# Kernel tuning notes

Hardware: AMD Instinct MI355X
Metric: run time of the kernel (lower is better)

The kernel has to match this reference:

```python
import jax, jax.numpy as jnp
import numpy as np

N, K, A, LOCAL, PAIR = 1024, 48, 5, 512, 128
RBF_BINS = 16

def _normalize(v, eps=1e-8):
    return v / jnp.sqrt(jnp.sum(v * v, axis=-1, keepdims=True) + eps)

def _frames(pos):
    # pos: (N, A, 3); backbone frame from N(0), CA(1), C(2) via Gram-Schmidt
    n, ca, c = pos[:, 0], pos[:, 1], pos[:, 2]
    e1 = _normalize(c - ca)
    v2 = n - ca
    e2 = _normalize(v2 - jnp.sum(v2 * e1, -1, keepdims=True) * e1)
    e3 = jnp.cross(e1, e2)
    R = jnp.stack([e1, e2, e3], axis=-1)  # (N,3,3) columns are frame axes
    return R, ca

def _rbf(d, d_min=0.0, d_max=22.0, bins=RBF_BINS):
    centers = jnp.linspace(d_min, d_max, bins)
    step = (d_max - d_min) / bins
    return jnp.exp(-((d[..., None] - centers) / step) ** 2)

def setup_inputs():
    key = jax.random.key(0)
    ks = jax.random.split(key, 16)
    def rn(k, shape, scale=1.0):
        return (scale * jax.random.normal(k, shape)).astype(jnp.float32)
    local = rn(ks[0], (N, LOCAL))
    pos = rn(ks[1], (N, A, 3), 3.0)
    pair = rn(ks[2], (N, N, PAIR), 0.1)
    neighbours = jax.random.randint(ks[3], (N, K), 0, N).astype(jnp.int32)
    mask = jnp.ones((N,), dtype=bool)
    d_dist = A * A * RBF_BINS   # 400
    d_dir = A * A * 3           # 75
    d_vec = 2 * A * 3           # 30
    s = lambda f: 1.0 / np.sqrt(f)
    return dict(
        local=local, pos=pos, pair=pair, neighbours=neighbours, mask=mask,
        W_li=rn(ks[4], (LOCAL, PAIR), s(LOCAL)),
        W_lj=rn(ks[5], (LOCAL, PAIR), s(LOCAL)),
        W_dist=rn(ks[6], (d_dist, PAIR), s(d_dist)),
        W_dir=rn(ks[7], (d_dir, PAIR), s(d_dir)),
        W_rot=rn(ks[8], (9, PAIR), s(9)),
        W_vec=rn(ks[9], (d_vec, PAIR), s(d_vec)),
        ln_scale=jnp.ones((PAIR,), jnp.float32),
        ln_bias=jnp.zeros((PAIR,), jnp.float32),
        mlp_w1=rn(ks[10], (PAIR, 2 * PAIR), s(PAIR)),
        mlp_b1=jnp.zeros((2 * PAIR,), jnp.float32),
        mlp_w2=rn(ks[11], (2 * PAIR, PAIR), s(2 * PAIR)),
        mlp_b2=jnp.zeros((PAIR,), jnp.float32),
    )

def reference(local, pos, pair, neighbours, mask,
              W_li, W_lj, W_dist, W_dir, W_rot, W_vec,
              ln_scale, ln_bias, mlp_w1, mlp_b1, mlp_w2, mlp_b2):
    n_idx = jnp.arange(neighbours.shape[0])
    pair_mask = (mask[:, None] & mask[neighbours]) & (neighbours != -1)
    p = pair[n_idx[:, None], neighbours]                      # (N,K,PAIR) gather
    R, t = _frames(pos)                                       # (N,3,3), (N,3)
    pos_nb = pos[neighbours]                                  # (N,K,A,3)
    # source / target node feature projections
    p = p + (local @ W_li)[:, None] + (local @ W_lj)[neighbours]
    # distance features: all atom-pair distances, RBF-encoded in [0, 22]
    off = pos[:, None, :, None, :] - pos_nb[:, :, None, :, :] # (N,K,A,A,3)
    dist = jnp.sqrt(jnp.sum(off * off, -1) + 1e-8)            # (N,K,A,A)
    p = p + _rbf(dist).reshape(*neighbours.shape, -1) @ W_dist
    # direction features: atom-pair offsets in the local frame, normalized
    off_local = jnp.einsum('nij,nkabi->nkabj', R, off)
    p = p + _normalize(off_local).reshape(*neighbours.shape, -1) @ W_dir
    # relative rotation features: R_i^T R_j, flattened
    R_rel = jnp.einsum('nai,nkaj->nkij', R, R[neighbours])
    p = p + R_rel.reshape(*neighbours.shape, 9) @ W_rot
    # pair vector features: self and neighbour atoms in the local frame (x0.1)
    x_self = jnp.einsum('nij,nai->naj', R, pos - t[:, None])            # (N,A,3)
    x_nb = jnp.einsum('nij,nkai->nkaj', R, pos_nb - t[:, None, None])   # (N,K,A,3)
    vec = jnp.concatenate(
        (0.1 * jnp.broadcast_to(x_self[:, None], x_nb.shape), 0.1 * x_nb),
        axis=-1).reshape(*neighbours.shape, -1)
    p = p + vec @ W_vec
    # LayerNorm (scale + offset)
    mu = jnp.mean(p, -1, keepdims=True)
    var = jnp.var(p, -1, keepdims=True)
    p = (p - mu) * jax.lax.rsqrt(var + 1e-5) * ln_scale + ln_bias
    # MLP: hidden 2*PAIR, gelu, linear out
    p = jax.nn.gelu(p @ mlp_w1 + mlp_b1) @ mlp_w2 + mlp_b2
    return p, pair_mask
```

## Files before the change

kernel.cpp:

```cpp
#include <hip/hip_runtime.h>
#include <hip/hip_bf16.h>
#include <math.h>

#define N 1024
#define K 48
#define A 5
#define LOCALD 512
#define PAIRD 128
#define ROWS 32
#define FEATK 544
#define SF_STRIDE_B 1152

#define WS_LI (N*9 + N*3 + N*15)
#define WS_LJ (WS_LI + N*128)
#define WCT_OFF 1159168u
#define W1T_OFF 1298432u
#define W2T_OFF 1363968u

typedef _Float16 half8 __attribute__((ext_vector_type(8)));
typedef float f32x16 __attribute__((ext_vector_type(16)));

__device__ __forceinline__ float gelu_fast(float x) {
    float u2 = 1.5957691216057308f * x * (1.0f + 0.044715f * x * x);
    float t = __expf(-u2);
    return x * __builtin_amdgcn_rcpf(1.0f + t);
}

__device__ __forceinline__ void frame_from(const float* __restrict__ P, float* __restrict__ R) {
    float e1x = P[6] - P[3], e1y = P[7] - P[4], e1z = P[8] - P[5];
    float inv1 = rsqrtf(e1x * e1x + e1y * e1y + e1z * e1z + 1e-8f);
    e1x *= inv1; e1y *= inv1; e1z *= inv1;
    float v2x = P[0] - P[3], v2y = P[1] - P[4], v2z = P[2] - P[5];
    float dp = v2x * e1x + v2y * e1y + v2z * e1z;
    float e2x = v2x - dp * e1x, e2y = v2y - dp * e1y, e2z = v2z - dp * e1z;
    float inv2 = rsqrtf(e2x * e2x + e2y * e2y + e2z * e2z + 1e-8f);
    e2x *= inv2; e2y *= inv2; e2z *= inv2;
    float e3x = e1y * e2z - e1z * e2y;
    float e3y = e1z * e2x - e1x * e2z;
    float e3z = e1x * e2y - e1y * e2x;
    R[0] = e1x; R[1] = e2x; R[2] = e3x;
    R[3] = e1y; R[4] = e2y; R[5] = e3y;
    R[6] = e1z; R[7] = e2z; R[8] = e3z;
}

__global__ __launch_bounds__(256) void prep_kernel(
    const float* __restrict__ local_,
    const float* __restrict__ W_li, const float* __restrict__ W_lj,
    const float* __restrict__ Wd, const float* __restrict__ Wdir,
    const float* __restrict__ Wrot, const float* __restrict__ Wv,
    const float* __restrict__ w1, const float* __restrict__ w2,
    float* __restrict__ ws, char* __restrict__ wsb)
{
    const int tid = threadIdx.x;
    if (blockIdx.x >= 256) {
        _Float16* wct = (_Float16*)(wsb + WCT_OFF);
        _Float16* w1t = (_Float16*)(wsb + W1T_OFF);
        _Float16* w2t = (_Float16*)(wsb + W2T_OFF);
        int g = (blockIdx.x - 256) * 256 + tid;
        if (g < 128 * 544) {
            int c = g & 127, f = g >> 7;
            float v = 0.0f;
            if (f < 400) v = Wd[(size_t)f * 128 + c];
            else if (f < 475) v = Wdir[(size_t)(f - 400) * 128 + c];
            else if (f < 484) v = Wrot[(size_t)(f - 475) * 128 + c];
            else if (f < 514) v = Wv[(size_t)(f - 484) * 128 + c];
            wct[(size_t)c * FEATK + f] = (_Float16)v;
        } else {
            int g2 = g - 128 * 544;
            if (g2 < 256 * 128) {
                int c = g2 & 255, f = g2 >> 8;
                w1t[(size_t)c * 128 + f] = (_Float16)w1[(size_t)f * 256 + c];
            } else {
                int g3 = g2 - 256 * 128;
                if (g3 < 128 * 256) {
                    int c = g3 & 127, f = g3 >> 7;
                    w2t[(size_t)c * 256 + f] = (_Float16)w2[(size_t)f * 128 + c];
                }
            }
        }
        return;
    }

    const int n0 = blockIdx.x * 4;
    __shared__ float sl[4][LOCALD];
    for (int t = tid; t < 4 * LOCALD; t += 256) {
        int r = t >> 9, q = t & 511;
        sl[r][q] = local_[(size_t)(n0 + r) * LOCALD + q];
    }
    __syncthreads();

    const int c = tid & 127;
    const int hh = tid >> 7;
    const int r0 = hh * 2;
    float ali0 = 0, ali1 = 0, alj0 = 0, alj1 = 0;
    const float* wli = W_li + c;
    const float* wlj = W_lj + c;
    #pragma unroll 8
    for (int f = 0; f < LOCALD; ++f) {
        float a_ = wli[(size_t)f * 128];
        float b_ = wlj[(size_t)f * 128];
        float l0 = sl[r0 + 0][f], l1 = sl[r0 + 1][f];
        ali0 += l0 * a_; ali1 += l1 * a_;
        alj0 += l0 * b_; alj1 += l1 * b_;
    }
    ws[WS_LI + (size_t)(n0 + r0 + 0) * 128 + c] = ali0;
    ws[WS_LI + (size_t)(n0 + r0 + 1) * 128 + c] = ali1;
    ws[WS_LJ + (size_t)(n0 + r0 + 0) * 128 + c] = alj0;
    ws[WS_LJ + (size_t)(n0 + r0 + 1) * 128 + c] = alj1;
}

__device__ __forceinline__ void sfw(char* smem, int r, int f, float v) {
    int off = r * SF_STRIDE_B + ((f * 2) ^ ((r & 7) << 4));
    *(_Float16*)(smem + off) = (_Float16)v;
}

__global__ __launch_bounds__(256, 4) void main_kernel(
    const float* __restrict__ pair, const float* __restrict__ pos,
    const int* __restrict__ neigh, const int* __restrict__ mask,
    const float* __restrict__ ln_s, const float* __restrict__ ln_b,
    const float* __restrict__ b1, const float* __restrict__ b2,
    const float* __restrict__ ws, const char* __restrict__ wsb,
    float* __restrict__ out)
{
    const int R0 = blockIdx.x * ROWS;
    const int tid = threadIdx.x;
    const int lane = tid & 63;
    const int wv = tid >> 6;
    const int myrow = lane & 31;
    const int khalf = (lane >> 5) * 8;
    const int hi = lane >> 5;
    const int swz = (myrow & 7) << 4;

    __shared__ __align__(16) char smem[40960];
    int*   sn  = (int*)(smem + 36864);
    int*   sj  = (int*)(smem + 36992);
    float* spn = (float*)(smem + 37120);
    float* spj = (float*)(smem + 39040);

    const _Float16* wct = (const _Float16*)(wsb + WCT_OFF);
    const int colbase = wv * 32 + myrow;

    if (tid < ROWS) {
        int Rg = R0 + tid;
        int n = Rg / K;
        int kk = Rg - n * K;
        int j = neigh[n * K + kk];
        if (j < 0) j += N;
        sn[tid] = n; sj[tid] = j;
    }
    __syncthreads();

    const int nb0 = R0 / K;
    const int nb1 = (nb0 + 1 < N) ? nb0 + 1 : nb0;
    float li0 = ws[WS_LI + (size_t)nb0 * PAIRD + colbase];
    float li1 = ws[WS_LI + (size_t)nb1 * PAIRD + colbase];
    float pv[16];
    #pragma unroll
    for (int q = 0; q < 16; ++q) {
        int rr = (q & 3) + 8 * (q >> 2) + 4 * hi;
        int nq = sn[rr], jq = sj[rr];
        float li = (nq == nb0) ? li0 : li1;
        pv[q] = pair[((size_t)nq * N + jq) * PAIRD + colbase]
              + ws[WS_LJ + (size_t)jq * PAIRD + colbase] + li;
    }

    for (int t = tid; t < ROWS * 15; t += 256) {
        int r = t / 15, q = t % 15;
        spn[t] = pos[(size_t)sn[r] * 15 + q];
        spj[t] = pos[(size_t)sj[r] * 15 + q];
    }
    __syncthreads();

    {
        const int fr  = tid >> 3;
        const int sub = tid & 7;
        const float* Pn = spn + fr * 15;
        const float* Pj = spj + fr * 15;

        sfw(smem, fr, 514 + sub, 0.0f);
        sfw(smem, fr, 522 + sub, 0.0f);
        sfw(smem, fr, 530 + sub, 0.0f);
        if (sub < 6) sfw(smem, fr, 538 + sub, 0.0f);

        float rn[9];
        frame_from(Pn, rn);

        #pragma unroll
        for (int m = 0; m < 4; ++m) {
            int ab = sub + 8 * m;
            if (ab < 25) {
                int a = ab / 5, b = ab - 5 * (ab / 5);
                float o0 = Pn[a * 3 + 0] - Pj[b * 3 + 0];
                float o1 = Pn[a * 3 + 1] - Pj[b * 3 + 1];
                float o2 = Pn[a * 3 + 2] - Pj[b * 3 + 2];
                float d = sqrtf(o0 * o0 + o1 * o1 + o2 * o2 + 1e-8f);
                float z = d * (16.0f / 22.0f);
                int base = a * 80 + b * 16;
                int rb = fr * SF_STRIDE_B;
                int rsw = (fr & 7) << 4;
                #pragma unroll
                for (int bp = 0; bp < 8; ++bp) {
                    float e0 = __expf(-z * z);
                    float z1 = z - 1.0666666666666667f;
                    float e1 = __expf(-z1 * z1);
                    z = z1 - 1.0666666666666667f;
                    union { _Float16 h[2]; unsigned u; } pk;
                    pk.h[0] = (_Float16)e0; pk.h[1] = (_Float16)e1;
                    int off = rb + (((base + bp * 2) * 2) ^ rsw);
                    *(unsigned*)(smem + off) = pk.u;
                }
                float l0 = rn[0] * o0 + rn[3] * o1 + rn[6] * o2;
                float l1 = rn[1] * o0 + rn[4] * o1 + rn[7] * o2;
                float l2 = rn[2] * o0 + rn[5] * o1 + rn[8] * o2;
                float inv = rsqrtf(l0 * l0 + l1 * l1 + l2 * l2 + 1e-8f);
                int dbase = 400 + a * 15 + b * 3;
                sfw(smem, fr, dbase + 0, l0 * inv);
                sfw(smem, fr, dbase + 1, l1 * inv);
                sfw(smem, fr, dbase + 2, l2 * inv);
            }
        }

        #pragma unroll
        for (int m = 0; m < 2; ++m) {
            int task = (m == 0) ? sub : (sub < 2 ? 8 + sub : -1);
            if (task >= 0) {
                int a = task >> 1;
                int kind = task & 1;
                const float* Ps = kind ? Pj : Pn;
                float v0 = Ps[a * 3 + 0] - Pn[3];
                float v1 = Ps[a * 3 + 1] - Pn[4];
                float v2 = Ps[a * 3 + 2] - Pn[5];
                float x0 = rn[0] * v0 + rn[3] * v1 + rn[6] * v2;
                float x1 = rn[1] * v0 + rn[4] * v1 + rn[7] * v2;
                float x2 = rn[2] * v0 + rn[5] * v1 + rn[8] * v2;
                int dbase = 484 + a * 6 + kind * 3;
                sfw(smem, fr, dbase + 0, 0.1f * x0);
                sfw(smem, fr, dbase + 1, 0.1f * x1);
                sfw(smem, fr, dbase + 2, 0.1f * x2);
            }
        }

        if (sub == 7) {
            float rj[9];
            frame_from(Pj, rj);
            #pragma unroll
            for (int i = 0; i < 3; ++i)
                #pragma unroll
                for (int jd = 0; jd < 3; ++jd) {
                    float v = rn[0 * 3 + i] * rj[0 * 3 + jd]
                            + rn[1 * 3 + i] * rj[1 * 3 + jd]
                            + rn[2 * 3 + i] * rj[2 * 3 + jd];
                    sfw(smem, fr, 475 + i * 3 + jd, v);
                }
        }
    }
    __syncthreads();

    f32x16 acc0, acc1;
    #pragma unroll
    for (int q = 0; q < 16; ++q) { acc0[q] = 0.0f; acc1[q] = 0.0f; }
    {
        const _Float16* wp = wct + (size_t)colbase * FEATK + khalf;
        #pragma unroll
        for (int ks = 0; ks < 34; ks += 2) {
            half8 b0 = *(const half8*)(wp + ks * 16);
            half8 b1 = *(const half8*)(wp + (ks + 1) * 16);
            int k0 = ks * 16 + khalf;
            int k1 = (ks + 1) * 16 + khalf;
            half8 a0 = *(const half8*)(smem + myrow * SF_STRIDE_B + ((k0 * 2) ^ swz));
            half8 a1 = *(const half8*)(smem + myrow * SF_STRIDE_B + ((k1 * 2) ^ swz));
            acc0 = __builtin_amdgcn_mfma_f32_32x32x16_f16(a0, b0, acc0, 0, 0, 0);
            acc1 = __builtin_amdgcn_mfma_f32_32x32x16_f16(a1, b1, acc1, 0, 0, 0);
        }
    }
    __syncthreads();

    #pragma unroll
    for (int q = 0; q < 16; ++q) {
        int rr = (q & 3) + 8 * (q >> 2) + 4 * hi;
        *(float*)(smem + rr * 512 + colbase * 4) = acc0[q] + acc1[q] + pv[q];
    }
    __syncthreads();

    {
        float lns0 = ln_s[lane], lns1 = ln_s[lane + 64];
        float lnb0 = ln_b[lane], lnb1 = ln_b[lane + 64];
        #pragma unroll
        for (int rr8 = 0; rr8 < 8; ++rr8) {
            int row = wv * 8 + rr8;
            float v0 = *(float*)(smem + row * 512 + lane * 4);
            float v1 = *(float*)(smem + row * 512 + (lane + 64) * 4);
            float s = v0 + v1, s2 = v0 * v0 + v1 * v1;
            #pragma unroll
            for (int o = 32; o > 0; o >>= 1) {
                s += __shfl_xor(s, o, 64);
                s2 += __shfl_xor(s2, o, 64);
            }
            float mu = s * (1.0f / 128.0f);
            float var = s2 * (1.0f / 128.0f) - mu * mu;
            float rs = rsqrtf(var + 1e-5f);
            int sw = (row & 7) << 4;
            *(_Float16*)(smem + 16384 + row * 256 + ((lane * 2) ^ sw)) =
                (_Float16)((v0 - mu) * rs * lns0 + lnb0);
            *(_Float16*)(smem + 16384 + row * 256 + (((lane + 64) * 2) ^ sw)) =
                (_Float16)((v1 - mu) * rs * lns1 + lnb1);
        }
    }
    __syncthreads();

    {
        const _Float16* w1t = (const _Float16*)(wsb + W1T_OFF);
        const int c0 = wv * 64 + myrow;
        const int c1 = c0 + 32;
        const _Float16* wp0 = w1t + (size_t)c0 * 128 + khalf;
        const _Float16* wp1 = w1t + (size_t)c1 * 128 + khalf;
        f32x16 h0, h1;
        #pragma unroll
        for (int q = 0; q < 16; ++q) { h0[q] = 0.0f; h1[q] = 0.0f; }
        #pragma unroll
        for (int ks = 0; ks < 8; ++ks) {
            half8 wf0 = *(const half8*)(wp0 + ks * 16);
            half8 wf1 = *(const half8*)(wp1 + ks * 16);
            int k0 = ks * 16 + khalf;
            half8 a = *(const half8*)(smem + 16384 + myrow * 256 + ((k0 * 2) ^ swz));
            h0 = __builtin_amdgcn_mfma_f32_32x32x16_f16(a, wf0, h0, 0, 0, 0);
            h1 = __builtin_amdgcn_mfma_f32_32x32x16_f16(a, wf1, h1, 0, 0, 0);
        }
        float bb0 = b1[c0], bb1 = b1[c1];
        #pragma unroll
        for (int q = 0; q < 16; ++q) {
            int rr = (q & 3) + 8 * (q >> 2) + 4 * hi;
            int sw = (rr & 7) << 4;
            *(_Float16*)(smem + rr * 512 + ((c0 * 2) ^ sw)) = (_Float16)gelu_fast(h0[q] + bb0);
            *(_Float16*)(smem + rr * 512 + ((c1 * 2) ^ sw)) = (_Float16)gelu_fast(h1[q] + bb1);
        }
    }
    __syncthreads();

    {
        const _Float16* w2t = (const _Float16*)(wsb + W2T_OFF);
        const int oc = wv * 32 + myrow;
        const _Float16* wp = w2t + (size_t)oc * 256 + khalf;
        f32x16 o0, o1;
        #pragma unroll
        for (int q = 0; q < 16; ++q) { o0[q] = 0.0f; o1[q] = 0.0f; }
        #pragma unroll
        for (int ks = 0; ks < 16; ks += 2) {
            half8 w0 = *(const half8*)(wp + ks * 16);
            half8 w1f = *(const half8*)(wp + (ks + 1) * 16);
            int k0 = ks * 16 + khalf;
            int k1 = (ks + 1) * 16 + khalf;
            half8 a0 = *(const half8*)(smem + myrow * 512 + ((k0 * 2) ^ swz));
            half8 a1 = *(const half8*)(smem + myrow * 512 + ((k1 * 2) ^ swz));
            o0 = __builtin_amdgcn_mfma_f32_32x32x16_f16(a0, w0, o0, 0, 0, 0);
            o1 = __builtin_amdgcn_mfma_f32_32x32x16_f16(a1, w1f, o1, 0, 0, 0);
        }
        float bb = b2[oc];
        #pragma unroll
        for (int q = 0; q < 16; ++q) {
            int rr = (q & 3) + 8 * (q >> 2) + 4 * hi;
            out[((size_t)(R0 + rr)) * PAIRD + oc] = o0[q] + o1[q] + bb;
        }
    }

    if (tid < ROWS) {
        int Rg = R0 + tid;
        int n = Rg / K;
        int kk = Rg - n * K;
        int jr = neigh[n * K + kk];
        int jj = jr < 0 ? jr + N : jr;
        bool pm = (jr != -1) && (mask[n] != 0) && (mask[jj] != 0);
        out[(size_t)N * K * PAIRD + Rg] = pm ? 1.0f : 0.0f;
    }
}

extern "C" void kernel_launch(void* const* d_in, const int* in_sizes, int n_in,
                              void* d_out, int out_size, void* d_ws, size_t ws_size,
                              hipStream_t stream) {
    const float* local_ = (const float*)d_in[0];
    const float* pos = (const float*)d_in[1];
    const float* pair = (const float*)d_in[2];
    const int* neigh = (const int*)d_in[3];
    const int* mask = (const int*)d_in[4];
    const float* W_li = (const float*)d_in[5];
    const float* W_lj = (const float*)d_in[6];
    const float* W_dist = (const float*)d_in[7];
    const float* W_dir = (const float*)d_in[8];
    const float* W_rot = (const float*)d_in[9];
    const float* W_vec = (const float*)d_in[10];
    const float* ln_s = (const float*)d_in[11];
    const float* ln_b = (const float*)d_in[12];
    const float* w1 = (const float*)d_in[13];
    const float* b1 = (const float*)d_in[14];
    const float* w2 = (const float*)d_in[15];
    const float* b2 = (const float*)d_in[16];
    float* ws = (float*)d_ws;
    char* wsb = (char*)d_ws;
    float* out = (float*)d_out;

    hipLaunchKernelGGL(prep_kernel, dim3(256 + 528), dim3(256), 0, stream,
                       local_, W_li, W_lj, W_dist, W_dir, W_rot, W_vec,
                       w1, w2, ws, wsb);
    hipLaunchKernelGGL(main_kernel, dim3((N * K) / ROWS), dim3(256), 0, stream,
                       pair, pos, neigh, mask, ln_s, ln_b, b1, b2, ws, wsb, out);
}
```

Measured before the change: 83.75 us.

## Split MLP into separate 64-row kernel via fp16 workspace intermediate

The fused kernel now stops after LayerNorm and writes normalized fp16 rows to a workspace buffer. A new mlp_kernel processes 64 rows per block, so each loaded weight fragment feeds two MFMA row tiles. This roughly halves weight traffic per row and lets the MLP run at its own occupancy. In exchange it adds a global round trip of about 12.6 MB of fp16 activations and an extra launch, and it falls back to the fused path when the workspace is too small.

New measurement: 80.09 us. 4.4% less time.

```diff
diff --git a/kernel.cpp b/kernel.cpp
--- a/kernel.cpp
+++ b/kernel.cpp
@@ -16,6 +16,8 @@
 #define WCT_OFF 1159168u
 #define W1T_OFF 1298432u
 #define W2T_OFF 1363968u
+#define PA_OFF  1429504u
+#define WS_NEEDED (1429504ull + 49152ull*128*2)
 
 typedef _Float16 half8 __attribute__((ext_vector_type(8)));
 typedef float f32x16 __attribute__((ext_vector_type(16)));
@@ -114,21 +116,22 @@
     *(_Float16*)(smem + off) = (_Float16)v;
 }
 
+template<bool SPLIT>
 __global__ __launch_bounds__(256, 4) void main_kernel(
     const float* __restrict__ pair, const float* __restrict__ pos,
     const int* __restrict__ neigh, const int* __restrict__ mask,
     const float* __restrict__ ln_s, const float* __restrict__ ln_b,
     const float* __restrict__ b1, const float* __restrict__ b2,
     const float* __restrict__ ws, const char* __restrict__ wsb,
-    float* __restrict__ out)
+    _Float16* __restrict__ pa, float* __restrict__ out)
 {
     const int R0 = blockIdx.x * ROWS;
     const int tid = threadIdx.x;
     const int lane = tid & 63;
     const int wv = tid >> 6;
     const int myrow = lane & 31;
-    const int khalf = (lane >> 5) * 8;
     const int hi = lane >> 5;
+    const int khalf = hi * 8;
     const int swz = (myrow & 7) << 4;
 
     __shared__ __align__(16) char smem[40960];
@@ -299,13 +302,20 @@
             float mu = s * (1.0f / 128.0f);
             float var = s2 * (1.0f / 128.0f) - mu * mu;
             float rs = rsqrtf(var + 1e-5f);
-            int sw = (row & 7) << 4;
-            *(_Float16*)(smem + 16384 + row * 256 + ((lane * 2) ^ sw)) =
-                (_Float16)((v0 - mu) * rs * lns0 + lnb0);
-            *(_Float16*)(smem + 16384 + row * 256 + (((lane + 64) * 2) ^ sw)) =
-                (_Float16)((v1 - mu) * rs * lns1 + lnb1);
-        }
-    }
+            float y0 = (v0 - mu) * rs * lns0 + lnb0;
+            float y1 = (v1 - mu) * rs * lns1 + lnb1;
+            if constexpr (SPLIT) {
+                pa[(size_t)(R0 + row) * PAIRD + lane]      = (_Float16)y0;
+                pa[(size_t)(R0 + row) * PAIRD + lane + 64] = (_Float16)y1;
+            } else {
+                int sw = (row & 7) << 4;
+                *(_Float16*)(smem + 16384 + row * 256 + ((lane * 2) ^ sw)) = (_Float16)y0;
+                *(_Float16*)(smem + 16384 + row * 256 + (((lane + 64) * 2) ^ sw)) = (_Float16)y1;
+            }
+        }
+    }
+    if constexpr (SPLIT) return;
+
     __syncthreads();
 
     {
@@ -364,6 +374,100 @@
     }
 
     if (tid < ROWS) {
+        int Rg = R0 + tid;
+        int n = Rg / K;
+        int kk = Rg - n * K;
+        int jr = neigh[n * K + kk];
+        int jj = jr < 0 ? jr + N : jr;
+        bool pm = (jr != -1) && (mask[n] != 0) && (mask[jj] != 0);
+        out[(size_t)N * K * PAIRD + Rg] = pm ? 1.0f : 0.0f;
+    }
+}
+
+__global__ __launch_bounds__(256, 3) void mlp_kernel(
+    const _Float16* __restrict__ pa, const int* __restrict__ neigh,
+    const int* __restrict__ mask, const float* __restrict__ b1,
+    const float* __restrict__ b2, const char* __restrict__ wsb,
+    float* __restrict__ out)
+{
+    const int R0 = blockIdx.x * 64;
+    const int tid = threadIdx.x;
+    const int lane = tid & 63;
+    const int wv = tid >> 6;
+    const int myrow = lane & 31;
+    const int hi = lane >> 5;
+    const int khalf = hi * 8;
+    const int swz = (myrow & 7) << 4;
+
+    __shared__ __align__(16) char smem[49152];
+
+    for (int ch = tid; ch < 1024; ch += 256) {
+        int row = ch >> 4, c16 = ch & 15;
+        half8 v = *(const half8*)(pa + (size_t)(R0 + row) * PAIRD + c16 * 8);
+        *(half8*)(smem + row * 256 + ((c16 * 16) ^ ((row & 7) << 4))) = v;
+    }
+    __syncthreads();
+
+    {
+        const _Float16* w1t = (const _Float16*)(wsb + W1T_OFF);
+        const int c0 = wv * 64 + myrow;
+        const int c1 = c0 + 32;
+        const _Float16* wp0 = w1t + (size_t)c0 * 128 + khalf;
+        const _Float16* wp1 = w1t + (size_t)c1 * 128 + khalf;
+        f32x16 h00, h01, h10, h11;
+        #pragma unroll
+        for (int q = 0; q < 16; ++q) { h00[q] = 0.0f; h01[q] = 0.0f; h10[q] = 0.0f; h11[q] = 0.0f; }
+        #pragma unroll
+        for (int ks = 0; ks < 8; ++ks) {
+            int k0 = ks * 16 + khalf;
+            half8 wf0 = *(const half8*)(wp0 + ks * 16);
+            half8 wf1 = *(const half8*)(wp1 + ks * 16);
+            half8 a0 = *(const half8*)(smem + myrow * 256 + ((k0 * 2) ^ swz));
+            half8 a1 = *(const half8*)(smem + (32 + myrow) * 256 + ((k0 * 2) ^ swz));
+            h00 = __builtin_amdgcn_mfma_f32_32x32x16_f16(a0, wf0, h00, 0, 0, 0);
+            h01 = __builtin_amdgcn_mfma_f32_32x32x16_f16(a0, wf1, h01, 0, 0, 0);
+            h10 = __builtin_amdgcn_mfma_f32_32x32x16_f16(a1, wf0, h10, 0, 0, 0);
+            h11 = __builtin_amdgcn_mfma_f32_32x32x16_f16(a1, wf1, h11, 0, 0, 0);
+        }
+        float bb0 = b1[c0], bb1 = b1[c1];
+        #pragma unroll
+        for (int q = 0; q < 16; ++q) {
+            int rr = (q & 3) + 8 * (q >> 2) + 4 * hi;
+            int sw = (rr & 7) << 4;
+            *(_Float16*)(smem + 16384 + rr * 512 + ((c0 * 2) ^ sw)) = (_Float16)gelu_fast(h00[q] + bb0);
+            *(_Float16*)(smem + 16384 + rr * 512 + ((c1 * 2) ^ sw)) = (_Float16)gelu_fast(h01[q] + bb1);
+            *(_Float16*)(smem + 16384 + (rr + 32) * 512 + ((c0 * 2) ^ sw)) = (_Float16)gelu_fast(h10[q] + bb0);
+            *(_Float16*)(smem + 16384 + (rr + 32) * 512 + ((c1 * 2) ^ sw)) = (_Float16)gelu_fast(h11[q] + bb1);
+        }
+    }
+    __syncthreads();
+
+    {
+        const _Float16* w2t = (const _Float16*)(wsb + W2T_OFF);
+        const int oc = wv * 32 + myrow;
+        const _Float16* wp = w2t + (size_t)oc * 256 + khalf;
+        f32x16 o0, o1;
+        #pragma unroll
+        for (int q = 0; q < 16; ++q) { o0[q] = 0.0f; o1[q] = 0.0f; }
+        #pragma unroll
+        for (int ks = 0; ks < 16; ++ks) {
+            int k0 = ks * 16 + khalf;
+            half8 wf = *(const half8*)(wp + ks * 16);
+            half8 a0 = *(const half8*)(smem + 16384 + myrow * 512 + ((k0 * 2) ^ swz));
+            half8 a1 = *(const half8*)(smem + 16384 + (32 + myrow) * 512 + ((k0 * 2) ^ swz));
+            o0 = __builtin_amdgcn_mfma_f32_32x32x16_f16(a0, wf, o0, 0, 0, 0);
+            o1 = __builtin_amdgcn_mfma_f32_32x32x16_f16(a1, wf, o1, 0, 0, 0);
+        }
+        float bb = b2[oc];
+        #pragma unroll
+        for (int q = 0; q < 16; ++q) {
+            int rr = (q & 3) + 8 * (q >> 2) + 4 * hi;
+            out[((size_t)(R0 + rr)) * PAIRD + oc]      = o0[q] + bb;
+            out[((size_t)(R0 + rr + 32)) * PAIRD + oc] = o1[q] + bb;
+        }
+    }
+
+    if (tid < 64) {
         int Rg = R0 + tid;
         int n = Rg / K;
         int kk = Rg - n * K;
@@ -396,11 +500,19 @@
     const float* b2 = (const float*)d_in[16];
     float* ws = (float*)d_ws;
     char* wsb = (char*)d_ws;
+    _Float16* pa = (_Float16*)(wsb + PA_OFF);
     float* out = (float*)d_out;
 
     hipLaunchKernelGGL(prep_kernel, dim3(256 + 528), dim3(256), 0, stream,
                        local_, W_li, W_lj, W_dist, W_dir, W_rot, W_vec,
                        w1, w2, ws, wsb);
-    hipLaunchKernelGGL(main_kernel, dim3((N * K) / ROWS), dim3(256), 0, stream,
-                       pair, pos, neigh, mask, ln_s, ln_b, b1, b2, ws, wsb, out);
-}
+    if (ws_size >= WS_NEEDED) {
+        main_kernel<true><<<dim3((N * K) / ROWS), dim3(256), 0, stream>>>(
+            pair, pos, neigh, mask, ln_s, ln_b, b1, b2, ws, wsb, pa, out);
+        mlp_kernel<<<dim3((N * K) / 64), dim3(256), 0, stream>>>(
+            pa, neigh, mask, b1, b2, wsb, out);
+    } else {
+        main_kernel<false><<<dim3((N * K) / ROWS), dim3(256), 0, stream>>>(
+            pair, pos, neigh, mask, ln_s, ln_b, b1, b2, ws, wsb, pa, out);
+    }
+}
```
